# Kernel tuning notes

Hardware: AMD Instinct MI355X
Metric: run time of the kernel (lower is better)

The kernel has to match this reference:

```python
import jax, jax.numpy as jnp
import numpy as np

EMBED = 256; HEADS = 8; LEVELS = 4; POINTS = 4; HEAD_DIM = EMBED // HEADS
B = 2; Q = 20000; HP = 128; WP = 128
EPS = 1e-5


def setup_inputs() -> dict:
    key = jax.random.key(0)
    ks = jax.random.split(key, 12)
    s = 1.0 / np.sqrt(EMBED)
    return {
        "query": jax.random.normal(ks[0], (Q, EMBED), jnp.float32),
        "query_spatial_positions": jax.random.uniform(ks[1], (Q, 2), jnp.float32),
        "query_batch_offsets": jnp.array([0, Q // 2, Q], dtype=jnp.int32),
        "stacked_feature_maps": jax.random.normal(ks[2], (B, HP, WP, LEVELS, EMBED), jnp.float32),
        "level_spatial_shapes": jnp.array([[128, 128], [64, 64], [32, 32], [16, 16]], dtype=jnp.int32),
        "norm_gamma": jnp.ones((EMBED,), jnp.float32),
        "norm_beta": jnp.zeros((EMBED,), jnp.float32),
        "W_q": jax.random.normal(ks[3], (EMBED, EMBED), jnp.float32) * s,
        "W_off": jax.random.normal(ks[4], (EMBED, HEADS * LEVELS * POINTS * 2), jnp.float32) * s * 0.1,
        "b_off": jax.random.normal(ks[5], (HEADS * LEVELS * POINTS * 2,), jnp.float32) * 0.5,
        "W_attn": jax.random.normal(ks[6], (EMBED, HEADS * LEVELS * POINTS), jnp.float32) * s,
        "b_attn": jnp.zeros((HEADS * LEVELS * POINTS,), jnp.float32),
        "W_val": jax.random.normal(ks[7], (EMBED, EMBED), jnp.float32) * s,
        "b_val": jnp.zeros((EMBED,), jnp.float32),
        "W_out": jax.random.normal(ks[8], (EMBED, EMBED), jnp.float32) * s,
    }


def _layernorm(x, g, b):
    mu = x.mean(-1, keepdims=True)
    xc = x - mu
    v = (xc * xc).mean(-1, keepdims=True)
    return xc * jax.lax.rsqrt(v + EPS) * g + b


def reference(query, query_spatial_positions, query_batch_offsets, stacked_feature_maps,
              level_spatial_shapes, norm_gamma, norm_beta, W_q, W_off, b_off,
              W_attn, b_attn, W_val, b_val, W_out):
    residual = query
    x = _layernorm(query, norm_gamma, norm_beta)
    x = x @ W_q  # q_in_proj (no bias)

    off = (x @ W_off + b_off).reshape(Q, HEADS, LEVELS, POINTS, 2)
    attn = jax.nn.softmax((x @ W_attn + b_attn).reshape(Q, HEADS, LEVELS * POINTS), axis=-1)
    attn = attn.reshape(Q, HEADS, LEVELS, POINTS)

    # value projection over all levels, split into heads: [B,HP,WP,L,H,HD]
    value = (stacked_feature_maps @ W_val + b_val).reshape(B, HP, WP, LEVELS, HEADS, HEAD_DIM)

    shp = level_spatial_shapes.astype(jnp.float32)  # [L,2] (h,w)
    # normalized ref point + offset scaled by level size -> pixel coords (align_corners=False)
    loc = query_spatial_positions[:, None, None, None, :] + off / shp[None, None, :, None, :]
    pix = loc * shp[None, None, :, None, :] - 0.5  # [Q,H,L,P,2]
    py, px = pix[..., 0], pix[..., 1]
    y0 = jnp.floor(py); x0 = jnp.floor(px)
    wy = py - y0; wx = px - x0
    y0i = y0.astype(jnp.int32); x0i = x0.astype(jnp.int32)

    Hl = level_spatial_shapes[:, 0][None, None, :, None]
    Wl = level_spatial_shapes[:, 1][None, None, :, None]
    b_idx = (jnp.searchsorted(query_batch_offsets, jnp.arange(Q, dtype=jnp.int32), side='right') - 1)[:, None, None, None]
    l_idx = jnp.arange(LEVELS)[None, None, :, None]
    h_idx = jnp.arange(HEADS)[None, :, None, None]

    def gather(yi, xi, w):
        m = (yi >= 0) & (yi < Hl) & (xi >= 0) & (xi < Wl)  # zero-pad outside level extent
        yc = jnp.clip(yi, 0, HP - 1)
        xc = jnp.clip(xi, 0, WP - 1)
        v = value[b_idx, yc, xc, l_idx, h_idx]  # [Q,H,L,P,HD]
        return v * (w * m)[..., None]

    samp = (gather(y0i, x0i, (1 - wy) * (1 - wx))
            + gather(y0i, x0i + 1, (1 - wy) * wx)
            + gather(y0i + 1, x0i, wy * (1 - wx))
            + gather(y0i + 1, x0i + 1, wy * wx))

    out = (attn[..., None] * samp).sum(axis=(2, 3)).reshape(Q, EMBED)
    return out @ W_out + residual
```

## Files before the change

### kernel.cpp

```cpp
#include <hip/hip_runtime.h>
#include <hip/hip_bf16.h>
#include <stdint.h>

#define EMBED 256
#define HEADS 8
#define LEVELS 4
#define POINTS 4
#define HEAD_DIM 32
#define HPAD 128
#define WPAD 128
#define LN_EPS 1e-5f

typedef unsigned short u16;
typedef __attribute__((ext_vector_type(8))) short bf16x8v;
typedef __attribute__((ext_vector_type(4))) float f32x4;

static __device__ __forceinline__ float bu2f(u16 u) {
  return __uint_as_float(((unsigned)u) << 16);
}
static __device__ __forceinline__ u16 f2bu(float f) {
  unsigned x = __float_as_uint(f);
  return (u16)((x + 0x7fffu + ((x >> 16) & 1u)) >> 16);
}
static __device__ __forceinline__ float loadf(const void* p, size_t i, int isbf) {
  return isbf ? bu2f(((const u16*)p)[i]) : ((const float*)p)[i];
}
static __device__ __forceinline__ int imin(int a, int b) { return a < b ? a : b; }

__global__ __launch_bounds__(256) void detect_kernel(const unsigned* __restrict__ q,
                                                     int* __restrict__ flag) {
  int t = threadIdx.x;
  __shared__ int s[256];
  unsigned u = q[t * 13 + 1];
  unsigned e = (u >> 7) & 0xFF;
  s[t] = (e >= 116 && e <= 130) ? 1 : 0;
  __syncthreads();
  for (int st = 128; st > 0; st >>= 1) { if (t < st) s[t] += s[t + st]; __syncthreads(); }
  if (t == 0) *flag = (s[0] > 200) ? 1 : 0;
}

__global__ __launch_bounds__(384) void boa_kernel(const void* __restrict__ b_off,
                                                  const void* __restrict__ b_attn,
                                                  float* __restrict__ boa,
                                                  const int* __restrict__ dflag) {
  int fl = *dflag;
  int t = threadIdx.x;
  boa[t] = (t < 256) ? loadf(b_off, t, fl) : loadf(b_attn, t - 256, fl);
}

__global__ __launch_bounds__(256) void bfold1_kernel(const void* __restrict__ beta,
                                                     const void* __restrict__ Wq,
                                                     float* __restrict__ t1,
                                                     const int* __restrict__ dflag) {
  int fl = *dflag;
  int j = threadIdx.x;
  float s = 0.f;
  for (int k = 0; k < 256; k++) s += loadf(beta, k, fl) * loadf(Wq, (size_t)k * 256 + j, fl);
  t1[j] = s;
}

__global__ __launch_bounds__(384) void bfold2_kernel(const float* __restrict__ t1,
                                                     const void* __restrict__ Woff,
                                                     const void* __restrict__ Wattn,
                                                     float* __restrict__ boa,
                                                     const int* __restrict__ dflag) {
  int fl = *dflag;
  int n = threadIdx.x;
  float s = 0.f;
  if (n < 256) { for (int j = 0; j < 256; j++) s += t1[j] * loadf(Woff,  (size_t)j * 256 + n,        fl); }
  else         { for (int j = 0; j < 256; j++) s += t1[j] * loadf(Wattn, (size_t)j * 128 + (n - 256), fl); }
  boa[n] += s;
}

__global__ __launch_bounds__(1024) void wcomb_kernel(const void* __restrict__ Wq,
                                                     const void* __restrict__ Woff,
                                                     const void* __restrict__ Wattn,
                                                     const void* __restrict__ gamma,
                                                     u16* __restrict__ Wt,
                                                     const int* __restrict__ dflag) {
  int fl = *dflag;
  int n0 = blockIdx.x * 32, k0 = blockIdx.y * 32;
  int tx = threadIdx.x & 31;
  int ty = threadIdx.x >> 5;
  __shared__ float Aq[32][33];
  __shared__ float Bo[32][33];
  float acc = 0.f;
  for (int j0 = 0; j0 < 256; j0 += 32) {
    Aq[ty][tx] = loadf(Wq, (size_t)(k0 + ty) * 256 + j0 + tx, fl);
    int n = n0 + tx;
    Bo[ty][tx] = (n < 256) ? loadf(Woff,  (size_t)(j0 + ty) * 256 + n,        fl)
                           : loadf(Wattn, (size_t)(j0 + ty) * 128 + (n - 256), fl);
    __syncthreads();
#pragma unroll
    for (int j = 0; j < 32; j++) acc += Aq[ty][j] * Bo[j][tx];
    __syncthreads();
  }
  acc *= loadf(gamma, k0 + ty, fl);
  Wt[(size_t)(n0 + tx) * 256 + k0 + ty] = f2bu(acc);
}

__global__ __launch_bounds__(256) void wtrans_kernel(const void* __restrict__ W,
                                                     u16* __restrict__ Wt,
                                                     int K, int N,
                                                     const int* __restrict__ dflag) {
  int fl = *dflag;
  __shared__ float tile[32][33];
  int tx = threadIdx.x & 31, ty = threadIdx.x >> 5;
  int k0 = blockIdx.x * 32, n0 = blockIdx.y * 32;
#pragma unroll
  for (int j = 0; j < 4; j++) {
    int r = ty + j * 8;
    tile[r][tx] = loadf(W, (size_t)(k0 + r) * N + n0 + tx, fl);
  }
  __syncthreads();
#pragma unroll
  for (int j = 0; j < 4; j++) {
    int n = ty + j * 8;
    Wt[(size_t)(n0 + n) * K + k0 + tx] = f2bu(tile[tx][n]);
  }
}

template <int OUTMODE, bool DOLN>
__global__ __launch_bounds__(512) void fullk_gemm(const void* __restrict__ A,
                                                  const u16* __restrict__ Bt,
                                                  const float* __restrict__ bias,
                                                  const void* __restrict__ resid,
                                                  void* __restrict__ Cv,
                                                  int M, int NB,
                                                  const int* __restrict__ dflag) {
  int fl = *dflag;
  __shared__ u16 As[128 * 256];
  int tid = threadIdx.x;
  int m0 = blockIdx.x * 128;
  int wave = tid >> 6, lane = tid & 63;
  int quad = lane >> 4, r16 = lane & 15;
  int wm = (wave >> 2) * 64, wn = (wave & 3) * 32;
  const int N = NB * 128;

  if (DOLN) {
    int r = tid >> 2, qt = tid & 3;
    int ra = imin(m0 + r, M - 1);
    if (fl) {
      uint4 d[8];
      const uint4* Ar = (const uint4*)((const u16*)A + (size_t)ra * 256 + qt * 64);
#pragma unroll
      for (int i = 0; i < 8; i++) d[i] = Ar[i];
      float s = 0.f;
#pragma unroll
      for (int i = 0; i < 8; i++) {
        unsigned w0 = d[i].x, w1 = d[i].y, w2 = d[i].z, w3 = d[i].w;
        s += __uint_as_float(w0 << 16) + __uint_as_float(w0 & 0xffff0000u)
           + __uint_as_float(w1 << 16) + __uint_as_float(w1 & 0xffff0000u)
           + __uint_as_float(w2 << 16) + __uint_as_float(w2 & 0xffff0000u)
           + __uint_as_float(w3 << 16) + __uint_as_float(w3 & 0xffff0000u);
      }
      s += __shfl_xor(s, 1, 64); s += __shfl_xor(s, 2, 64);
      float mu = s * (1.f / 256.f);
      float sq = 0.f;
#pragma unroll
      for (int i = 0; i < 8; i++) {
        unsigned w0 = d[i].x, w1 = d[i].y, w2 = d[i].z, w3 = d[i].w;
        float c;
        c = __uint_as_float(w0 << 16) - mu; sq += c * c;
        c = __uint_as_float(w0 & 0xffff0000u) - mu; sq += c * c;
        c = __uint_as_float(w1 << 16) - mu; sq += c * c;
        c = __uint_as_float(w1 & 0xffff0000u) - mu; sq += c * c;
        c = __uint_as_float(w2 << 16) - mu; sq += c * c;
        c = __uint_as_float(w2 & 0xffff0000u) - mu; sq += c * c;
        c = __uint_as_float(w3 << 16) - mu; sq += c * c;
        c = __uint_as_float(w3 & 0xffff0000u) - mu; sq += c * c;
      }
      sq += __shfl_xor(sq, 1, 64); sq += __shfl_xor(sq, 2, 64);
      float rr = rsqrtf(sq * (1.f / 256.f) + LN_EPS);
#pragma unroll
      for (int i = 0; i < 8; i++) {
        unsigned w[4] = {d[i].x, d[i].y, d[i].z, d[i].w};
        uint4 o;
        unsigned* op = &o.x;
#pragma unroll
        for (int k = 0; k < 4; k++) {
          float lo = (__uint_as_float(w[k] << 16) - mu) * rr;
          float hi = (__uint_as_float(w[k] & 0xffff0000u) - mu) * rr;
          op[k] = (unsigned)f2bu(lo) | ((unsigned)f2bu(hi) << 16);
        }
        int c = qt * 8 + i;
        *(uint4*)&As[r * 256 + ((c ^ (r & 7)) * 8)] = o;
      }
    } else {
      const float4* Ar4 = (const float4*)((const float*)A + (size_t)ra * 256 + qt * 64);
      float s = 0.f, sq = 0.f;
#pragma unroll
      for (int i = 0; i < 16; i++) {
        float4 f = Ar4[i];
        s  += f.x + f.y + f.z + f.w;
        sq += f.x * f.x + f.y * f.y + f.z * f.z + f.w * f.w;
      }
      s  += __shfl_xor(s, 1, 64);  s  += __shfl_xor(s, 2, 64);
      sq += __shfl_xor(sq, 1, 64); sq += __shfl_xor(sq, 2, 64);
      float mu = s * (1.f / 256.f);
      float var = sq * (1.f / 256.f) - mu * mu;
      float rr = rsqrtf(fmaxf(var, 0.f) + LN_EPS);
#pragma unroll
      for (int i = 0; i < 16; i += 2) {
        float4 f0 = Ar4[i], f1 = Ar4[i + 1];
        uint4 o;
        o.x = (unsigned)f2bu((f0.x - mu) * rr) | ((unsigned)f2bu((f0.y - mu) * rr) << 16);
        o.y = (unsigned)f2bu((f0.z - mu) * rr) | ((unsigned)f2bu((f0.w - mu) * rr) << 16);
        o.z = (unsigned)f2bu((f1.x - mu) * rr) | ((unsigned)f2bu((f1.y - mu) * rr) << 16);
        o.w = (unsigned)f2bu((f1.z - mu) * rr) | ((unsigned)f2bu((f1.w - mu) * rr) << 16);
        int c = qt * 8 + (i >> 1);
        *(uint4*)&As[r * 256 + ((c ^ (r & 7)) * 8)] = o;
      }
    }
  } else {
    const uint4* A16 = (const uint4*)A;
#pragma unroll
    for (int it = 0; it < 8; it++) {
      int g = it * 512 + tid;
      int r = g >> 5, c = g & 31;
      int ra = imin(m0 + r, M - 1);
      uint4 v = A16[(size_t)ra * 32 + c];
      *(uint4*)&As[r * 256 + ((c ^ (r & 7)) * 8)] = v;
    }
  }
  __syncthreads();

  int arow[4], arl[4];
#pragma unroll
  for (int i = 0; i < 4; i++) {
    int rw = wm + i * 16 + r16;
    arow[i] = rw * 256;
    arl[i]  = rw & 7;
  }

  int obf = (OUTMODE == 2) ? fl : OUTMODE;
  int sl0 = (quad << 4) | ((2 * r16) & 15);
  int sl1 = sl0 + 1;
  bool lohalf = (r16 < 8);

  for (int nb = 0; nb < NB; ++nb) {
    f32x4 acc[4][2];
#pragma unroll
    for (int i = 0; i < 4; i++) { acc[i][0] = (f32x4){0.f,0.f,0.f,0.f}; acc[i][1] = (f32x4){0.f,0.f,0.f,0.f}; }
    const u16* bb0 = Bt + (size_t)(nb * 128 + wn + r16) * 256 + quad * 8;
    const u16* bb1 = bb0 + 16 * 256;
#pragma unroll
    for (int t = 0; t < 8; t++) {
      bf16x8v b0 = *(const bf16x8v*)(bb0 + t * 32);
      bf16x8v b1 = *(const bf16x8v*)(bb1 + t * 32);
#pragma unroll
      for (int i = 0; i < 4; i++) {
        int chunk = ((t << 2) | quad) ^ arl[i];
        bf16x8v a = *(const bf16x8v*)&As[arow[i] + chunk * 8];
        acc[i][0] = __builtin_amdgcn_mfma_f32_16x16x32_bf16(a, b0, acc[i][0], 0, 0, 0);
        acc[i][1] = __builtin_amdgcn_mfma_f32_16x16x32_bf16(a, b1, acc[i][1], 0, 0, 0);
      }
    }
    if (bias) {
      float bv0 = bias[nb * 128 + wn + r16];
      float bv1 = bias[nb * 128 + wn + 16 + r16];
#pragma unroll
      for (int i = 0; i < 4; i++)
#pragma unroll
        for (int reg = 0; reg < 4; reg++) { acc[i][0][reg] += bv0; acc[i][1][reg] += bv1; }
    }
    if (obf) {
#pragma unroll
      for (int i = 0; i < 4; i++) {
#pragma unroll
        for (int reg = 0; reg < 4; reg++) {
          float vA = acc[i][0][reg], vB = acc[i][1][reg];
          float a0 = __shfl(vA, sl0), a1 = __shfl(vA, sl1);
          float b0s = __shfl(vB, sl0), b1s = __shfl(vB, sl1);
          float lo = lohalf ? a0 : b0s;
          float hi = lohalf ? a1 : b1s;
          int row = m0 + wm + i * 16 + quad * 4 + reg;
          if (row < M) {
            size_t base = (size_t)row * N + nb * 128 + wn + 2 * r16;
            if (resid) {
              lo += loadf(resid, base, fl);
              hi += loadf(resid, base + 1, fl);
            }
            unsigned pk = (unsigned)f2bu(lo) | ((unsigned)f2bu(hi) << 16);
            *(unsigned*)((u16*)Cv + base) = pk;
          }
        }
      }
    } else {
#pragma unroll
      for (int j = 0; j < 2; j++) {
        int col = nb * 128 + wn + j * 16 + r16;
#pragma unroll
        for (int i = 0; i < 4; i++) {
#pragma unroll
          for (int reg = 0; reg < 4; reg++) {
            int row = m0 + wm + i * 16 + quad * 4 + reg;
            if (row < M) {
              float v = acc[i][j][reg];
              if (resid) v += loadf(resid, (size_t)row * N + col, fl);
              ((float*)Cv)[(size_t)row * N + col] = v;
            }
          }
        }
      }
    }
  }
}

__global__ __launch_bounds__(512) void val_gemm(const void* __restrict__ A,
                                                const u16* __restrict__ Bt,
                                                const void* __restrict__ bias,
                                                u16* __restrict__ Cv,
                                                const int* __restrict__ dflag) {
  int fl = *dflag;
  __shared__ u16 As[128 * 256];
  int tid = threadIdx.x;
  int blk = blockIdx.x;
  int b   = blk / 170;
  int cb  = blk % 170;
  int l, ibase;
  if (cb < 128)      { l = 0; ibase = cb * 128; }
  else if (cb < 160) { l = 1; ibase = (cb - 128) * 128; }
  else if (cb < 168) { l = 2; ibase = (cb - 160) * 128; }
  else               { l = 3; ibase = (cb - 168) * 128; }
  int shift = 7 - l;
  int mask  = (128 >> l) - 1;
  int rowbase = b * 65536 + l;

  int wave = tid >> 6, lane = tid & 63;
  int quad = lane >> 4, r16 = lane & 15;
  int wm = (wave >> 2) * 64, wn = (wave & 3) * 64;

  if (fl) {
    const uint4* A16 = (const uint4*)A;
#pragma unroll
    for (int it = 0; it < 8; it++) {
      int g = it * 512 + tid;
      int r = g >> 5, c = g & 31;
      int i = ibase + r;
      size_t rowg = (size_t)rowbase + (i >> shift) * 512 + (i & mask) * 4;
      uint4 v = A16[rowg * 32 + c];
      *(uint4*)&As[r * 256 + ((c ^ (r & 7)) * 8)] = v;
    }
  } else {
    const float4* A4 = (const float4*)A;
#pragma unroll
    for (int p = 0; p < 2; p++) {
      float4 f[8];
#pragma unroll
      for (int q = 0; q < 8; q++) {
        int g = (p * 8 + q) * 512 + tid;
        int i = ibase + (g >> 6);
        size_t rowg = (size_t)rowbase + (i >> shift) * 512 + (i & mask) * 4;
        f[q] = A4[rowg * 64 + (g & 63)];
      }
#pragma unroll
      for (int q = 0; q < 8; q++) {
        int g = (p * 8 + q) * 512 + tid;
        int r = g >> 6, cw = g & 63;
        int c = cw >> 1, sub = cw & 1;
        uint2 w;
        w.x = (unsigned)f2bu(f[q].x) | ((unsigned)f2bu(f[q].y) << 16);
        w.y = (unsigned)f2bu(f[q].z) | ((unsigned)f2bu(f[q].w) << 16);
        *(uint2*)&As[r * 256 + ((c ^ (r & 7)) * 8) + sub * 4] = w;
      }
    }
  }
  __syncthreads();

  f32x4 acc[4][4];
#pragma unroll
  for (int i = 0; i < 4; i++)
#pragma unroll
    for (int j = 0; j < 4; j++) acc[i][j] = (f32x4){0.f, 0.f, 0.f, 0.f};

  int arow[4], arl[4];
#pragma unroll
  for (int i = 0; i < 4; i++) {
    arow[i] = (wm + i * 16 + r16) * 256;
    arl[i]  = (wm + i * 16 + r16) & 7;
  }
  const u16* bbase[4];
#pragma unroll
  for (int j = 0; j < 4; j++)
    bbase[j] = Bt + (size_t)(wn + j * 16 + r16) * 256 + quad * 8;

#pragma unroll
  for (int t = 0; t < 8; t++) {
    bf16x8v b4[4];
#pragma unroll
    for (int j = 0; j < 4; j++)
      b4[j] = *(const bf16x8v*)(bbase[j] + t * 32);
    bf16x8v a4[4];
#pragma unroll
    for (int i = 0; i < 4; i++) {
      int chunk = ((t << 2) | quad) ^ arl[i];
      a4[i] = *(const bf16x8v*)&As[arow[i] + chunk * 8];
    }
#pragma unroll
    for (int i = 0; i < 4; i++)
#pragma unroll
      for (int j = 0; j < 4; j++)
        acc[i][j] = __builtin_amdgcn_mfma_f32_16x16x32_bf16(a4[i], b4[j], acc[i][j], 0, 0, 0);
  }

#pragma unroll
  for (int j = 0; j < 4; j++) {
    float bv = loadf(bias, wn + j * 16 + r16, fl);
#pragma unroll
    for (int i = 0; i < 4; i++)
#pragma unroll
      for (int reg = 0; reg < 4; reg++) acc[i][j][reg] += bv;
  }
  int sl0 = (quad << 4) | ((2 * r16) & 15);
  int sl1 = sl0 + 1;
  bool lohalf = (r16 < 8);
#pragma unroll
  for (int i = 0; i < 4; i++) {
#pragma unroll
    for (int jp = 0; jp < 2; jp++) {
#pragma unroll
      for (int reg = 0; reg < 4; reg++) {
        float vA = acc[i][jp * 2][reg], vB = acc[i][jp * 2 + 1][reg];
        float a0 = __shfl(vA, sl0), a1 = __shfl(vA, sl1);
        float b0 = __shfl(vB, sl0), b1 = __shfl(vB, sl1);
        float lo = lohalf ? a0 : b0;
        float hi = lohalf ? a1 : b1;
        int rloc = wm + i * 16 + quad * 4 + reg;
        int ii = ibase + rloc;
        size_t rowg = (size_t)rowbase + (ii >> shift) * 512 + (ii & mask) * 4;
        size_t base = rowg * 256 + wn + jp * 32 + 2 * r16;
        unsigned pk = (unsigned)f2bu(lo) | ((unsigned)f2bu(hi) << 16);
        *(unsigned*)(Cv + base) = pk;
      }
    }
  }
}

__global__ __launch_bounds__(256) void sample2_kernel(const float* __restrict__ oa,
                                                      const void* __restrict__ qsp,
                                                      const int* __restrict__ qbo, int nb,
                                                      const int* __restrict__ lss,
                                                      const u16* __restrict__ value,
                                                      u16* __restrict__ samp, int Qn,
                                                      const int* __restrict__ dflag) {
  int fl = *dflag;
  int t = threadIdx.x;
  int q2 = t >> 7;
  int i7 = t & 127;
  int qb = blockIdx.x * 2;
  int q = imin(qb + q2, Qn - 1);

  __shared__ float Loff[2][256];
  __shared__ float Lw[2][128];
  __shared__ int   Lb[2];
  __shared__ int   Co[2][128][4];
  __shared__ float Cw[2][128][4];

  {
    const float* row = oa + (size_t)q * 384;
    float2 v = ((const float2*)row)[i7];
    Loff[q2][i7 * 2]     = v.x;
    Loff[q2][i7 * 2 + 1] = v.y;
    Lw[q2][i7] = row[256 + i7];
  }
  if (t < 2) {
    int qq = imin(qb + t, Qn - 1);
    int b = 0;
    for (int i = 1; i < nb; i++) if (qq >= qbo[i]) b = i;
    Lb[t] = b;
  }
  __syncthreads();

  if (t < 16) {
    int sq = t >> 3, h = t & 7;
    float* w = &Lw[sq][h * 16];
    float mx = w[0];
    for (int i = 1; i < 16; i++) mx = fmaxf(mx, w[i]);
    float s = 0.f;
    for (int i = 0; i < 16; i++) { float e = __expf(w[i] - mx); w[i] = e; s += e; }
    float inv = 1.f / s;
    for (int i = 0; i < 16; i++) w[i] *= inv;
  }
  __syncthreads();

  {
    int h = i7 >> 4, lp = i7 & 15, l = lp >> 2;
    int Hi = lss[l * 2], Wi = lss[l * 2 + 1];
    float Hl = (float)Hi, Wl = (float)Wi;
    float qy = loadf(qsp, (size_t)q * 2, fl);
    float qx = loadf(qsp, (size_t)q * 2 + 1, fl);
    float a  = Lw[q2][i7];
    float oy = Loff[q2][i7 * 2], ox = Loff[q2][i7 * 2 + 1];
    float py = (qy + oy / Hl) * Hl - 0.5f;
    float px = (qx + ox / Wl) * Wl - 0.5f;
    float y0f = floorf(py), x0f = floorf(px);
    float wy = py - y0f, wx = px - x0f;
    int y0 = (int)y0f, x0 = (int)x0f;
    int bbase = Lb[q2] * (HPAD * WPAD * LEVELS * EMBED);
#pragma unroll
    for (int c = 0; c < 4; c++) {
      int yi = y0 + (c >> 1), xi = x0 + (c & 1);
      float w = ((c >> 1) ? wy : 1.f - wy) * ((c & 1) ? wx : 1.f - wx);
      bool ok = (yi >= 0) & (yi < Hi) & (xi >= 0) & (xi < Wi);
      Co[q2][i7][c] = ok ? (bbase + ((yi * WPAD + xi) * LEVELS + l) * EMBED + h * HEAD_DIM) : 0;
      Cw[q2][i7][c] = ok ? (a * w) : 0.f;
    }
  }
  __syncthreads();

  {
    int h = (t >> 4) & 7;
    int d2 = t & 15;
    float ax = 0.f, ay = 0.f;
#pragma unroll
    for (int lp = 0; lp < 16; lp++) {
      int4   o4 = *(const int4*)&Co[q2][h * 16 + lp][0];
      float4 w4 = *(const float4*)&Cw[q2][h * 16 + lp][0];
      unsigned v;
      v = *(const unsigned*)(value + o4.x + d2 * 2);
      ax += w4.x * __uint_as_float(v << 16); ay += w4.x * __uint_as_float(v & 0xffff0000u);
      v = *(const unsigned*)(value + o4.y + d2 * 2);
      ax += w4.y * __uint_as_float(v << 16); ay += w4.y * __uint_as_float(v & 0xffff0000u);
      v = *(const unsigned*)(value + o4.z + d2 * 2);
      ax += w4.z * __uint_as_float(v << 16); ay += w4.z * __uint_as_float(v & 0xffff0000u);
      v = *(const unsigned*)(value + o4.w + d2 * 2);
      ax += w4.w * __uint_as_float(v << 16); ay += w4.w * __uint_as_float(v & 0xffff0000u);
    }
    if (qb + q2 < Qn) {
      unsigned pk = (unsigned)f2bu(ax) | ((unsigned)f2bu(ay) << 16);
      *(unsigned*)(samp + (size_t)(qb + q2) * 256 + h * 32 + d2 * 2) = pk;
    }
  }
}

extern "C" void kernel_launch(void* const* d_in, const int* in_sizes, int n_in,
                              void* d_out, int out_size, void* d_ws, size_t ws_size,
                              hipStream_t stream) {
  const void* query  = d_in[0];
  const void* qsp    = d_in[1];
  const int*  qbo    = (const int*)d_in[2];
  const void* sfm    = d_in[3];
  const int*  lss    = (const int*)d_in[4];
  const void* gamma  = d_in[5];
  const void* beta   = d_in[6];
  const void* W_q    = d_in[7];
  const void* W_off  = d_in[8];
  const void* b_off  = d_in[9];
  const void* W_attn = d_in[10];
  const void* b_attn = d_in[11];
  const void* W_val  = d_in[12];
  const void* b_val  = d_in[13];
  const void* W_out  = d_in[14];

  const int Q  = in_sizes[0] / EMBED;
  const int nb = in_sizes[2] - 1;
  const int MV = in_sizes[3] / EMBED;
  const int B  = MV / (HPAD * WPAD * LEVELS);

  char* ws = (char*)d_ws;
  size_t o = 0;
  auto alloc = [&](size_t bytes) { size_t r = o; o = (o + bytes + 255) & ~(size_t)255; return r; };
  float* oaw   = (float*)(ws + alloc((size_t)Q * 384 * sizeof(float)));
  u16*   valw  = (u16*)(ws + alloc((size_t)MV * EMBED * sizeof(u16)));
  u16*   sampw = (u16*)(ws + alloc((size_t)Q * EMBED * sizeof(u16)));
  u16*   wtoa  = (u16*)(ws + alloc(384 * 256 * sizeof(u16)));
  u16*   wtval = (u16*)(ws + alloc(256 * 256 * sizeof(u16)));
  u16*   wtout = (u16*)(ws + alloc(256 * 256 * sizeof(u16)));
  float* boa   = (float*)(ws + alloc(384 * sizeof(float)));
  float* t1    = (float*)(ws + alloc(256 * sizeof(float)));
  int*   dflag = (int*)(ws + alloc(256));
  (void)ws_size;

  detect_kernel<<<1, 256, 0, stream>>>((const unsigned*)query, dflag);
  boa_kernel<<<1, 384, 0, stream>>>(b_off, b_attn, boa, dflag);
  bfold1_kernel<<<1, 256, 0, stream>>>(beta, W_q, t1, dflag);
  bfold2_kernel<<<1, 384, 0, stream>>>(t1, W_off, W_attn, boa, dflag);

  wcomb_kernel<<<dim3(12, 8), 1024, 0, stream>>>(W_q, W_off, W_attn, gamma, wtoa, dflag);
  wtrans_kernel<<<dim3(8, 8), 256, 0, stream>>>(W_val, wtval, 256, 256, dflag);
  wtrans_kernel<<<dim3(8, 8), 256, 0, stream>>>(W_out, wtout, 256, 256, dflag);

  const int GQ = (Q + 127) / 128;
  fullk_gemm<0, true><<<GQ, 512, 0, stream>>>(query, wtoa, boa, nullptr, oaw, Q, 3, dflag);
  val_gemm<<<dim3(B * 170), 512, 0, stream>>>(sfm, wtval, b_val, valw, dflag);
  sample2_kernel<<<(Q + 1) / 2, 256, 0, stream>>>(oaw, qsp, qbo, nb, lss, valw, sampw, Q, dflag);
  fullk_gemm<2, false><<<GQ, 512, 0, stream>>>(sampw, wtout, nullptr, query, d_out, Q, 2, dflag);
}
```

Measured before the change: 464.2 us.

## Split LN+offset GEMM over N blocks and use async-LDS tiled GEMM for output

The fused LayerNorm+offset/attention GEMM now launches a 2D grid, one block per 128-column slice, instead of looping over three N-blocks inside one block. This raises parallelism but repeats the LayerNorm work for each slice. The output projection moves to a new 256-thread tiled MFMA GEMM that stages A and B through LDS in K-chunks of 32 using global_load_lds, with a 2D grid over N. The aim is better occupancy and load balance across CUs, at the cost of redundant row normalization and more per-K-step synchronization.

After: 466.7 us. Within noise of the previous version (+0.5%).

```diff
diff --git a/kernel.cpp b/kernel.cpp
--- a/kernel.cpp
+++ b/kernel.cpp
@@ -26,6 +26,11 @@
   return isbf ? bu2f(((const u16*)p)[i]) : ((const float*)p)[i];
 }
 static __device__ __forceinline__ int imin(int a, int b) { return a < b ? a : b; }
+
+static __device__ __forceinline__ void cp16(const u16* g, u16* l) {
+  __builtin_amdgcn_global_load_lds((const __attribute__((address_space(1))) unsigned*)g,
+                                   (__attribute__((address_space(3))) unsigned*)l, 16, 0, 0);
+}
 
 __global__ __launch_bounds__(256) void detect_kernel(const unsigned* __restrict__ q,
                                                      int* __restrict__ flag) {
@@ -120,24 +125,23 @@
   }
 }
 
-template <int OUTMODE, bool DOLN>
-__global__ __launch_bounds__(512) void fullk_gemm(const void* __restrict__ A,
-                                                  const u16* __restrict__ Bt,
-                                                  const float* __restrict__ bias,
-                                                  const void* __restrict__ resid,
-                                                  void* __restrict__ Cv,
-                                                  int M, int NB,
-                                                  const int* __restrict__ dflag) {
+__global__ __launch_bounds__(512) void lnoa_gemm(const void* __restrict__ A,
+                                                 const u16* __restrict__ Bt,
+                                                 const float* __restrict__ bias,
+                                                 float* __restrict__ Cv,
+                                                 int M,
+                                                 const int* __restrict__ dflag) {
   int fl = *dflag;
   __shared__ u16 As[128 * 256];
   int tid = threadIdx.x;
   int m0 = blockIdx.x * 128;
+  int noff = blockIdx.y * 128;
   int wave = tid >> 6, lane = tid & 63;
   int quad = lane >> 4, r16 = lane & 15;
   int wm = (wave >> 2) * 64, wn = (wave & 3) * 32;
-  const int N = NB * 128;
-
-  if (DOLN) {
+  const int N = 384;
+
+  {
     int r = tid >> 2, qt = tid & 3;
     int ra = imin(m0 + r, M - 1);
     if (fl) {
@@ -159,16 +163,13 @@
       float sq = 0.f;
 #pragma unroll
       for (int i = 0; i < 8; i++) {
-        unsigned w0 = d[i].x, w1 = d[i].y, w2 = d[i].z, w3 = d[i].w;
-        float c;
-        c = __uint_as_float(w0 << 16) - mu; sq += c * c;
-        c = __uint_as_float(w0 & 0xffff0000u) - mu; sq += c * c;
-        c = __uint_as_float(w1 << 16) - mu; sq += c * c;
-        c = __uint_as_float(w1 & 0xffff0000u) - mu; sq += c * c;
-        c = __uint_as_float(w2 << 16) - mu; sq += c * c;
-        c = __uint_as_float(w2 & 0xffff0000u) - mu; sq += c * c;
-        c = __uint_as_float(w3 << 16) - mu; sq += c * c;
-        c = __uint_as_float(w3 & 0xffff0000u) - mu; sq += c * c;
+        unsigned w[4] = {d[i].x, d[i].y, d[i].z, d[i].w};
+#pragma unroll
+        for (int k = 0; k < 4; k++) {
+          float c0 = __uint_as_float(w[k] << 16) - mu;
+          float c1 = __uint_as_float(w[k] & 0xffff0000u) - mu;
+          sq += c0 * c0 + c1 * c1;
+        }
       }
       sq += __shfl_xor(sq, 1, 64); sq += __shfl_xor(sq, 2, 64);
       float rr = rsqrtf(sq * (1.f / 256.f) + LN_EPS);
@@ -212,16 +213,6 @@
         *(uint4*)&As[r * 256 + ((c ^ (r & 7)) * 8)] = o;
       }
     }
-  } else {
-    const uint4* A16 = (const uint4*)A;
-#pragma unroll
-    for (int it = 0; it < 8; it++) {
-      int g = it * 512 + tid;
-      int r = g >> 5, c = g & 31;
-      int ra = imin(m0 + r, M - 1);
-      uint4 v = A16[(size_t)ra * 32 + c];
-      *(uint4*)&As[r * 256 + ((c ^ (r & 7)) * 8)] = v;
-    }
   }
   __syncthreads();
 
@@ -233,50 +224,126 @@
     arl[i]  = rw & 7;
   }
 
+  f32x4 acc[4][2];
+#pragma unroll
+  for (int i = 0; i < 4; i++) { acc[i][0] = (f32x4){0.f,0.f,0.f,0.f}; acc[i][1] = (f32x4){0.f,0.f,0.f,0.f}; }
+  const u16* bb0 = Bt + (size_t)(noff + wn + r16) * 256 + quad * 8;
+  const u16* bb1 = bb0 + 16 * 256;
+#pragma unroll
+  for (int t = 0; t < 8; t++) {
+    bf16x8v b0 = *(const bf16x8v*)(bb0 + t * 32);
+    bf16x8v b1 = *(const bf16x8v*)(bb1 + t * 32);
+#pragma unroll
+    for (int i = 0; i < 4; i++) {
+      int chunk = ((t << 2) | quad) ^ arl[i];
+      bf16x8v a = *(const bf16x8v*)&As[arow[i] + chunk * 8];
+      acc[i][0] = __builtin_amdgcn_mfma_f32_16x16x32_bf16(a, b0, acc[i][0], 0, 0, 0);
+      acc[i][1] = __builtin_amdgcn_mfma_f32_16x16x32_bf16(a, b1, acc[i][1], 0, 0, 0);
+    }
+  }
+  float bv0 = bias[noff + wn + r16];
+  float bv1 = bias[noff + wn + 16 + r16];
+#pragma unroll
+  for (int i = 0; i < 4; i++)
+#pragma unroll
+    for (int reg = 0; reg < 4; reg++) { acc[i][0][reg] += bv0; acc[i][1][reg] += bv1; }
+#pragma unroll
+  for (int j = 0; j < 2; j++) {
+    int col = noff + wn + j * 16 + r16;
+#pragma unroll
+    for (int i = 0; i < 4; i++) {
+#pragma unroll
+      for (int reg = 0; reg < 4; reg++) {
+        int row = m0 + wm + i * 16 + quad * 4 + reg;
+        if (row < M) Cv[(size_t)row * N + col] = acc[i][j][reg];
+      }
+    }
+  }
+}
+
+template <int OUTMODE, bool ABF>
+__global__ __launch_bounds__(256) void mfma_gemm(const void* __restrict__ A,
+                                                 const u16* __restrict__ Bt,
+                                                 const void* __restrict__ bias, int BiasC,
+                                                 const void* __restrict__ resid,
+                                                 void* __restrict__ Cv,
+                                                 int M, int N, int K,
+                                                 const int* __restrict__ dflag) {
+  int fl = *dflag;
+  __shared__ u16 As[4096];
+  __shared__ u16 Bs[4096];
+  int tid = threadIdx.x;
+  int m0 = blockIdx.x * 128, n0 = blockIdx.y * 128;
+  int wave = tid >> 6, lane = tid & 63;
+  int quad = lane >> 4, r16 = lane & 15;
+  int wm = (wave >> 1) * 64, wn = (wave & 1) * 64;
+
+  f32x4 acc[4][4];
+#pragma unroll
+  for (int i = 0; i < 4; i++)
+#pragma unroll
+    for (int j = 0; j < 4; j++) acc[i][j] = (f32x4){0.f, 0.f, 0.f, 0.f};
+
+  int p0 = tid, p1 = tid + 256;
+  int r0 = p0 >> 2, c0 = (p0 & 3) * 8;
+  int r1 = p1 >> 2, c1 = (p1 & 3) * 8;
+  int ra0 = imin(m0 + r0, M - 1), ra1 = imin(m0 + r1, M - 1);
+
+  const u16* Ab = (const u16*)A;
+
+  for (int k0 = 0; k0 < K; k0 += 32) {
+    __syncthreads();
+    cp16(Ab + (size_t)ra0 * K + k0 + c0, &As[p0 * 8]);
+    cp16(Ab + (size_t)ra1 * K + k0 + c1, &As[p1 * 8]);
+    cp16(Bt + (size_t)(n0 + r0) * K + k0 + c0, &Bs[p0 * 8]);
+    cp16(Bt + (size_t)(n0 + r1) * K + k0 + c1, &Bs[p1 * 8]);
+    __syncthreads();
+
+    bf16x8v a[4], b[4];
+#pragma unroll
+    for (int i = 0; i < 4; i++)
+      a[i] = *(const bf16x8v*)&As[(wm + i * 16 + r16) * 32 + quad * 8];
+#pragma unroll
+    for (int j = 0; j < 4; j++)
+      b[j] = *(const bf16x8v*)&Bs[(wn + j * 16 + r16) * 32 + quad * 8];
+#pragma unroll
+    for (int i = 0; i < 4; i++)
+#pragma unroll
+      for (int j = 0; j < 4; j++)
+        acc[i][j] = __builtin_amdgcn_mfma_f32_16x16x32_bf16(a[i], b[j], acc[i][j], 0, 0, 0);
+  }
+
   int obf = (OUTMODE == 2) ? fl : OUTMODE;
-  int sl0 = (quad << 4) | ((2 * r16) & 15);
-  int sl1 = sl0 + 1;
-  bool lohalf = (r16 < 8);
-
-  for (int nb = 0; nb < NB; ++nb) {
-    f32x4 acc[4][2];
-#pragma unroll
-    for (int i = 0; i < 4; i++) { acc[i][0] = (f32x4){0.f,0.f,0.f,0.f}; acc[i][1] = (f32x4){0.f,0.f,0.f,0.f}; }
-    const u16* bb0 = Bt + (size_t)(nb * 128 + wn + r16) * 256 + quad * 8;
-    const u16* bb1 = bb0 + 16 * 256;
-#pragma unroll
-    for (int t = 0; t < 8; t++) {
-      bf16x8v b0 = *(const bf16x8v*)(bb0 + t * 32);
-      bf16x8v b1 = *(const bf16x8v*)(bb1 + t * 32);
-#pragma unroll
-      for (int i = 0; i < 4; i++) {
-        int chunk = ((t << 2) | quad) ^ arl[i];
-        bf16x8v a = *(const bf16x8v*)&As[arow[i] + chunk * 8];
-        acc[i][0] = __builtin_amdgcn_mfma_f32_16x16x32_bf16(a, b0, acc[i][0], 0, 0, 0);
-        acc[i][1] = __builtin_amdgcn_mfma_f32_16x16x32_bf16(a, b1, acc[i][1], 0, 0, 0);
-      }
-    }
-    if (bias) {
-      float bv0 = bias[nb * 128 + wn + r16];
-      float bv1 = bias[nb * 128 + wn + 16 + r16];
+  if (bias) {
+    int bfl = (BiasC == 2) ? fl : 0;
+#pragma unroll
+    for (int j = 0; j < 4; j++) {
+      float bv = loadf(bias, n0 + wn + j * 16 + r16, bfl);
 #pragma unroll
       for (int i = 0; i < 4; i++)
 #pragma unroll
-        for (int reg = 0; reg < 4; reg++) { acc[i][0][reg] += bv0; acc[i][1][reg] += bv1; }
-    }
-    if (obf) {
-#pragma unroll
-      for (int i = 0; i < 4; i++) {
+        for (int reg = 0; reg < 4; reg++) acc[i][j][reg] += bv;
+    }
+  }
+
+  if (obf) {
+    int sl0 = (quad << 4) | ((2 * r16) & 15);
+    int sl1 = sl0 + 1;
+    bool lohalf = (r16 < 8);
+#pragma unroll
+    for (int i = 0; i < 4; i++) {
+#pragma unroll
+      for (int jp = 0; jp < 2; jp++) {
 #pragma unroll
         for (int reg = 0; reg < 4; reg++) {
-          float vA = acc[i][0][reg], vB = acc[i][1][reg];
+          float vA = acc[i][jp * 2][reg], vB = acc[i][jp * 2 + 1][reg];
           float a0 = __shfl(vA, sl0), a1 = __shfl(vA, sl1);
-          float b0s = __shfl(vB, sl0), b1s = __shfl(vB, sl1);
-          float lo = lohalf ? a0 : b0s;
-          float hi = lohalf ? a1 : b1s;
+          float b0 = __shfl(vB, sl0), b1 = __shfl(vB, sl1);
+          float lo = lohalf ? a0 : b0;
+          float hi = lohalf ? a1 : b1;
           int row = m0 + wm + i * 16 + quad * 4 + reg;
           if (row < M) {
-            size_t base = (size_t)row * N + nb * 128 + wn + 2 * r16;
+            size_t base = (size_t)row * N + n0 + wn + jp * 32 + 2 * r16;
             if (resid) {
               lo += loadf(resid, base, fl);
               hi += loadf(resid, base + 1, fl);
@@ -286,20 +353,20 @@
           }
         }
       }
-    } else {
-#pragma unroll
-      for (int j = 0; j < 2; j++) {
-        int col = nb * 128 + wn + j * 16 + r16;
-#pragma unroll
-        for (int i = 0; i < 4; i++) {
-#pragma unroll
-          for (int reg = 0; reg < 4; reg++) {
-            int row = m0 + wm + i * 16 + quad * 4 + reg;
-            if (row < M) {
-              float v = acc[i][j][reg];
-              if (resid) v += loadf(resid, (size_t)row * N + col, fl);
-              ((float*)Cv)[(size_t)row * N + col] = v;
-            }
+    }
+  } else {
+#pragma unroll
+    for (int j = 0; j < 4; j++) {
+      int col = n0 + wn + j * 16 + r16;
+#pragma unroll
+      for (int i = 0; i < 4; i++) {
+#pragma unroll
+        for (int reg = 0; reg < 4; reg++) {
+          int row = m0 + wm + i * 16 + quad * 4 + reg;
+          if (row < M) {
+            float v = acc[i][j][reg];
+            if (resid) v += loadf(resid, (size_t)row * N + col, fl);
+            ((float*)Cv)[(size_t)row * N + col] = v;
           }
         }
       }
@@ -582,8 +649,8 @@
   wtrans_kernel<<<dim3(8, 8), 256, 0, stream>>>(W_out, wtout, 256, 256, dflag);
 
   const int GQ = (Q + 127) / 128;
-  fullk_gemm<0, true><<<GQ, 512, 0, stream>>>(query, wtoa, boa, nullptr, oaw, Q, 3, dflag);
+  lnoa_gemm<<<dim3(GQ, 3), 512, 0, stream>>>(query, wtoa, boa, oaw, Q, dflag);
   val_gemm<<<dim3(B * 170), 512, 0, stream>>>(sfm, wtval, b_val, valw, dflag);
   sample2_kernel<<<(Q + 1) / 2, 256, 0, stream>>>(oaw, qsp, qbo, nb, lss, valw, sampw, Q, dflag);
-  fullk_gemm<2, false><<<GQ, 512, 0, stream>>>(sampw, wtout, nullptr, query, d_out, Q, 2, dflag);
-}
+  mfma_gemm<2, true><<<dim3(GQ, 2), 256, 0, stream>>>(sampw, wtout, nullptr, 0, query, d_out, Q, 256, 256, dflag);
+}
```
